# Kernel tuning notes

Measured on AMD Instinct MI355X. Metric: run time of the kernel, lower is better.

## Reference

```python
import jax, jax.numpy as jnp
import numpy as np

# AdaMem / network constants hardcoded in the torch module (mode='FULL')
BETA = 0.99        # membrane decay
THR_INIT = 1.0     # initial threshold (reset_mem)
SCALE = 5.0        # threshold adaptation jump per spike
THR_DECAY = 0.95   # threshold decay toward base
BASE_THR = 0.0     # base threshold
T = 200            # timesteps
B = 32             # batch
N_IN = 100 * 100   # fc1 input features
N_OUT = 3          # fc1 output features


def setup_inputs() -> dict:
    key = jax.random.key(0)
    k1, k2, k3, k4 = jax.random.split(key, 4)
    # sgen.rate: Bernoulli spikes with per-pixel probability = pixel intensity,
    # sampled independently at each of T timesteps -> [T, B, N_IN] in {0,1}
    intensity = jax.random.uniform(k1, (B, N_IN))
    spikes = (jax.random.uniform(k2, (T, B, N_IN)) < intensity).astype(jnp.float32)
    # fc1 parameters (Linear(10000, 3))
    W = jax.random.normal(k3, (N_OUT, N_IN), dtype=jnp.float32) * 0.01
    b = jax.random.normal(k4, (N_OUT,), dtype=jnp.float32) * 0.01
    return {"spikes": spikes, "W": W, "b": b}


def reference(spikes, W, b):
    # Batch all 200 independent linear projections into one GEMM: [T,B,N_IN] x [N_OUT,N_IN]
    proj = jnp.einsum('tbi,oi->tbo', spikes, W) + b  # [T, B, 3]

    def step(carry, x_t):
        mem, thr = carry
        mem = BETA * mem + x_t                       # leaky integration
        spk = (mem > thr).astype(mem.dtype)          # fire
        mem = mem - spk * thr                        # reset by subtraction
        thr = BASE_THR + THR_DECAY * (thr - BASE_THR) + SCALE * spk  # adaptive threshold
        return (mem, thr), (spk, mem)

    mem0 = jnp.zeros((B, N_OUT), dtype=proj.dtype)
    thr0 = jnp.full((B, N_OUT), THR_INIT, dtype=proj.dtype)
    _, (spk_rec, mem_rec) = jax.lax.scan(step, (mem0, thr0), proj)
    return spk_rec, mem_rec  # each [T, B, 3]
```

## Files before the change

### kernel.cpp

```cpp
#include <hip/hip_runtime.h>

#define T_STEPS 200
#define BATCH 32
#define N_IN 10000
#define N_OUT 3
#define ROWS (T_STEPS * BATCH)
#define STATES (BATCH * N_OUT)
#define PROJ_N (ROWS * N_OUT)
#define NV4 (N_IN / 4)
#define RPB 5

typedef float f32x4 __attribute__((ext_vector_type(4)));

__device__ __forceinline__ float dot4(f32x4 a, f32x4 b) {
    return a.x * b.x + a.y * b.y + a.z * b.z + a.w * b.w;
}

__global__ __launch_bounds__(256, 5) void proj_kernel(
    const float* __restrict__ spikes,
    const float* __restrict__ W,
    const float* __restrict__ bias,
    float* __restrict__ proj)
{
    const int row0 = blockIdx.x * RPB;
    const int tid = threadIdx.x;

    const f32x4* __restrict__ s0 = reinterpret_cast<const f32x4*>(spikes + (size_t)row0 * N_IN);
    const f32x4* __restrict__ W0 = reinterpret_cast<const f32x4*>(W);
    const f32x4* __restrict__ W1 = reinterpret_cast<const f32x4*>(W + N_IN);
    const f32x4* __restrict__ W2 = reinterpret_cast<const f32x4*>(W + 2 * N_IN);

    float acc[RPB][3];
    #pragma unroll
    for (int r = 0; r < RPB; ++r)
        #pragma unroll
        for (int o = 0; o < 3; ++o) acc[r][o] = 0.f;

    for (int i = tid; i < NV4; i += 256) {
        f32x4 s[RPB];
        #pragma unroll
        for (int r = 0; r < RPB; ++r)
            s[r] = s0[(size_t)r * NV4 + i];
        f32x4 w0 = W0[i];
        f32x4 w1 = W1[i];
        f32x4 w2 = W2[i];
        #pragma unroll
        for (int r = 0; r < RPB; ++r) {
            acc[r][0] += dot4(s[r], w0);
            acc[r][1] += dot4(s[r], w1);
            acc[r][2] += dot4(s[r], w2);
        }
    }

    #pragma unroll
    for (int r = 0; r < RPB; ++r)
        #pragma unroll
        for (int o = 0; o < 3; ++o)
            for (int off = 32; off > 0; off >>= 1)
                acc[r][o] += __shfl_down(acc[r][o], off);

    __shared__ float red[4][RPB][3];
    const int wave = tid >> 6;
    if ((tid & 63) == 0) {
        #pragma unroll
        for (int r = 0; r < RPB; ++r)
            #pragma unroll
            for (int o = 0; o < 3; ++o)
                red[wave][r][o] = acc[r][o];
    }
    __syncthreads();
    if (tid < RPB * 3) {
        const int r = tid / 3, o = tid % 3;
        float s = red[0][r][o] + red[1][r][o] + red[2][r][o] + red[3][r][o];
        proj[(size_t)(row0 + r) * 3 + o] = s + bias[o];
    }
}

__global__ __launch_bounds__(128) void scan_kernel(
    const float* __restrict__ proj,
    float* __restrict__ out)
{
    const int idx = threadIdx.x;
    if (idx >= STATES) return;

    float* __restrict__ spk_rec = out;
    float* __restrict__ mem_rec = out + PROJ_N;

    float mem = 0.0f;
    float thr = 1.0f;

    float xb[8];
    for (int t0 = 0; t0 < T_STEPS; t0 += 8) {
        #pragma unroll
        for (int k = 0; k < 8; ++k)
            xb[k] = proj[(size_t)(t0 + k) * STATES + idx];
        #pragma unroll
        for (int k = 0; k < 8; ++k) {
            mem = 0.99f * mem + xb[k];
            float spk = (mem > thr) ? 1.0f : 0.0f;
            mem -= spk * thr;
            thr = 0.95f * thr + 5.0f * spk;
            const int e = (t0 + k) * STATES + idx;
            spk_rec[e] = spk;
            mem_rec[e] = mem;
        }
    }
}

extern "C" void kernel_launch(void* const* d_in, const int* in_sizes, int n_in,
                              void* d_out, int out_size, void* d_ws, size_t ws_size,
                              hipStream_t stream) {
    const float* spikes = (const float*)d_in[0];
    const float* W      = (const float*)d_in[1];
    const float* b      = (const float*)d_in[2];
    float* out  = (float*)d_out;
    float* proj = (float*)d_ws;

    proj_kernel<<<ROWS / RPB, 256, 0, stream>>>(spikes, W, b, proj);
    scan_kernel<<<1, 128, 0, stream>>>(proj, out);
}
```

Before: 55.54 us.

## Fuse projection and scan via last-block atomic ticket, prefetch scan inputs

Merges the projection GEMV and the recurrent scan into one kernel. Each block takes an atomic ticket after writing its projections, and the last block to finish runs the scan. This removes the second kernel launch and its gap, at the cost of a memset on the stream and fences in every block. The scan now keeps two 8-step chunks of inputs loaded ahead of use, to hide global-load latency behind the serial recurrence.

```diff
diff --git a/kernel.cpp b/kernel.cpp
--- a/kernel.cpp
+++ b/kernel.cpp
@@ -9,6 +9,7 @@
 #define PROJ_N (ROWS * N_OUT)
 #define NV4 (N_IN / 4)
 #define RPB 5
+#define NBLK (ROWS / RPB)
 
 typedef float f32x4 __attribute__((ext_vector_type(4)));
 
@@ -16,11 +17,13 @@
     return a.x * b.x + a.y * b.y + a.z * b.z + a.w * b.w;
 }
 
-__global__ __launch_bounds__(256, 5) void proj_kernel(
+__global__ __launch_bounds__(256, 5) void fused_kernel(
     const float* __restrict__ spikes,
     const float* __restrict__ W,
     const float* __restrict__ bias,
-    float* __restrict__ proj)
+    float* __restrict__ proj,
+    unsigned* __restrict__ counter,
+    float* __restrict__ out)
 {
     const int row0 = blockIdx.x * RPB;
     const int tid = threadIdx.x;
@@ -74,13 +77,16 @@
         float s = red[0][r][o] + red[1][r][o] + red[2][r][o] + red[3][r][o];
         proj[(size_t)(row0 + r) * 3 + o] = s + bias[o];
     }
-}
 
-__global__ __launch_bounds__(128) void scan_kernel(
-    const float* __restrict__ proj,
-    float* __restrict__ out)
-{
-    const int idx = threadIdx.x;
+    __threadfence();
+    __syncthreads();
+    __shared__ unsigned s_ticket;
+    if (tid == 0) s_ticket = atomicAdd(counter, 1u);
+    __syncthreads();
+    if (s_ticket != NBLK - 1) return;
+    __threadfence();
+
+    const int idx = tid;
     if (idx >= STATES) return;
 
     float* __restrict__ spk_rec = out;
@@ -89,14 +95,19 @@
     float mem = 0.0f;
     float thr = 1.0f;
 
-    float xb[8];
+    float cur[8], n1[8], n2[8];
+    #pragma unroll
+    for (int k = 0; k < 8; ++k) cur[k] = proj[(size_t)(0 + k) * STATES + idx];
+    #pragma unroll
+    for (int k = 0; k < 8; ++k) n1[k] = proj[(size_t)(8 + k) * STATES + idx];
+
     for (int t0 = 0; t0 < T_STEPS; t0 += 8) {
+        const int tp = (t0 + 16 < T_STEPS) ? (t0 + 16) : 0;
         #pragma unroll
-        for (int k = 0; k < 8; ++k)
-            xb[k] = proj[(size_t)(t0 + k) * STATES + idx];
+        for (int k = 0; k < 8; ++k) n2[k] = proj[(size_t)(tp + k) * STATES + idx];
         #pragma unroll
         for (int k = 0; k < 8; ++k) {
-            mem = 0.99f * mem + xb[k];
+            mem = 0.99f * mem + cur[k];
             float spk = (mem > thr) ? 1.0f : 0.0f;
             mem -= spk * thr;
             thr = 0.95f * thr + 5.0f * spk;
@@ -104,6 +115,8 @@
             spk_rec[e] = spk;
             mem_rec[e] = mem;
         }
+        #pragma unroll
+        for (int k = 0; k < 8; ++k) { cur[k] = n1[k]; n1[k] = n2[k]; }
     }
 }
 
@@ -115,7 +128,8 @@
     const float* b      = (const float*)d_in[2];
     float* out  = (float*)d_out;
     float* proj = (float*)d_ws;
+    unsigned* counter = (unsigned*)((char*)d_ws + PROJ_N * sizeof(float));
 
-    proj_kernel<<<ROWS / RPB, 256, 0, stream>>>(spikes, W, b, proj);
-    scan_kernel<<<1, 128, 0, stream>>>(proj, out);
+    hipMemsetAsync(counter, 0, sizeof(unsigned), stream);
+    fused_kernel<<<NBLK, 256, 0, stream>>>(spikes, W, b, proj, counter, out);
 }
```

Result: slower. 190.6 us (+243.3%).
